# Kernel tuning notes

Hardware: AMD Instinct MI355X
Metric: run time of the kernel (lower is better)

The kernel has to match this reference:

```python
import jax, jax.numpy as jnp
import numpy as np

B, C, N = 8, 512, 2048
C2 = C // 2
BN_EPS = 1e-5


def setup_inputs() -> dict:
    key = jax.random.key(0)
    ks = jax.random.split(key, 8)
    s = lambda fan_in: 1.0 / np.sqrt(fan_in)
    return {
        "q": jax.random.normal(ks[0], (B, C, N), jnp.float32),
        "x": jax.random.normal(ks[1], (B, C2, N), jnp.float32),
        "Wq": jax.random.normal(ks[2], (C2, C), jnp.float32) * s(C),
        "Wk": jax.random.normal(ks[3], (C2, C2), jnp.float32) * s(C2),
        "Wv": jax.random.normal(ks[4], (C2, C), jnp.float32) * s(C),
        "bv": jax.random.normal(ks[5], (C2,), jnp.float32) * 0.01,
        "Wt": jax.random.normal(ks[6], (C2, C2), jnp.float32) * s(C2),
        "bt": jax.random.normal(ks[7], (C2,), jnp.float32) * 0.01,
        "gamma": jnp.ones((C2,), jnp.float32),
        "beta": jnp.zeros((C2,), jnp.float32),
        "running_mean": jnp.zeros((C2,), jnp.float32),
        "running_var": jnp.ones((C2,), jnp.float32),
    }


def reference(q, x, Wq, Wk, Wv, bv, Wt, bt, gamma, beta, running_mean, running_var):
    # 1x1 convs are pointwise GEMMs over the channel dim
    x_q = jnp.einsum("oc,bcn->bno", Wq, q)                    # [B, N, C2]
    x_k = jnp.einsum("oc,bcn->bon", Wk, x)                    # [B, C2, N]
    x_v = jnp.einsum("oc,bcn->bon", Wv, q) + bv[None, :, None]  # [B, C2, N]
    energy = jnp.einsum("bnc,bcm->bnm", x_q, x_k)             # [B, N, N]
    attn = jax.nn.softmax(energy, axis=-1)
    # offset-attention L1 renormalization over the query axis (dim=1)
    attn = attn / (1e-9 + attn.sum(axis=1, keepdims=True))
    x_r = jnp.einsum("bcn,bnm->bcm", x_v, attn)               # [B, C2, N]
    h = jnp.einsum("oc,bcn->bon", Wt, x - x_r) + bt[None, :, None]
    # BatchNorm1d in eval mode with running statistics
    inv = gamma / jnp.sqrt(running_var + BN_EPS)
    h = h * inv[None, :, None] + (beta - running_mean * inv)[None, :, None]
    return jax.nn.relu(h) + x
```

## Files before the change

kernel.cpp:

```cpp
#include <hip/hip_runtime.h>
#include <cstdint>
#include <cstddef>

#define KB_  8
#define KC_  512
#define KC2_ 256
#define KN_  2048

typedef __attribute__((ext_vector_type(8))) __bf16 bf16x8;
typedef __attribute__((ext_vector_type(8))) unsigned short u16x8;
typedef __attribute__((ext_vector_type(4))) float f32x4;

__device__ __forceinline__ unsigned short f2bf(float f) {
  union { float f; unsigned u; } x; x.f = f;
  unsigned r = x.u + 0x7fffu + ((x.u >> 16) & 1u);
  return (unsigned short)(r >> 16);
}
__device__ __forceinline__ float bf2f(unsigned short h) {
  union { unsigned u; float f; } x; x.u = ((unsigned)h) << 16;
  return x.f;
}

#define GLD16(g, l) __builtin_amdgcn_global_load_lds( \
    (__attribute__((address_space(1))) void*)(g),     \
    (__attribute__((address_space(3))) void*)(l), 16, 0, 0)

#define WAIT_VM8()  asm volatile("s_waitcnt vmcnt(8)" ::: "memory")
#define WAIT_VM0()  asm volatile("s_waitcnt vmcnt(0)" ::: "memory")
#define BARRIER()   __builtin_amdgcn_s_barrier()

__device__ __forceinline__ void xcd_swizzle(int& bx, int& by, int& bz) {
  const int gx = gridDim.x, gy = gridDim.y;
  const int nb = gx * gy * (int)gridDim.z;
  int f = ((int)blockIdx.z * gy + (int)blockIdx.y) * gx + (int)blockIdx.x;
  if ((nb & 7) == 0) f = (f & 7) * (nb >> 3) + (f >> 3);
  const int gxy = gx * gy;
  bz = f / gxy; int rem = f - bz * gxy;
  by = rem / gx; bx = rem - by * gx;
}

__global__ __launch_bounds__(256) void cvt_all_kernel(
    const float* __restrict__ Wq, const float* __restrict__ Wk,
    const float* __restrict__ Wv, const float* __restrict__ Wt,
    unsigned short* __restrict__ Wqhi, unsigned short* __restrict__ Wqlo,
    unsigned short* __restrict__ Wkhi, unsigned short* __restrict__ Wklo,
    unsigned short* __restrict__ Wvb, unsigned short* __restrict__ Wtb) {
  int blk = blockIdx.x, t = threadIdx.x;
  if (blk < 128) {
    int i = (blk * 256 + t) * 4;
    float4 f = *(const float4*)(Wq + i);
    ushort4 h = { f2bf(f.x), f2bf(f.y), f2bf(f.z), f2bf(f.w) };
    ushort4 l = { f2bf(f.x - bf2f(h.x)), f2bf(f.y - bf2f(h.y)),
                  f2bf(f.z - bf2f(h.z)), f2bf(f.w - bf2f(h.w)) };
    *(ushort4*)(Wqhi + i) = h; *(ushort4*)(Wqlo + i) = l;
  } else if (blk < 192) {
    int i = ((blk - 128) * 256 + t) * 4;
    float4 f = *(const float4*)(Wk + i);
    ushort4 h = { f2bf(f.x), f2bf(f.y), f2bf(f.z), f2bf(f.w) };
    ushort4 l = { f2bf(f.x - bf2f(h.x)), f2bf(f.y - bf2f(h.y)),
                  f2bf(f.z - bf2f(h.z)), f2bf(f.w - bf2f(h.w)) };
    *(ushort4*)(Wkhi + i) = h; *(ushort4*)(Wklo + i) = l;
  } else if (blk < 320) {
    int i = ((blk - 192) * 256 + t) * 4;
    float4 f = *(const float4*)(Wv + i);
    ushort4 u = { f2bf(f.x), f2bf(f.y), f2bf(f.z), f2bf(f.w) };
    *(ushort4*)(Wvb + i) = u;
  } else {
    int i = ((blk - 320) * 256 + t) * 4;
    float4 f = *(const float4*)(Wt + i);
    ushort4 u = { f2bf(f.x), f2bf(f.y), f2bf(f.z), f2bf(f.w) };
    *(ushort4*)(Wtb + i) = u;
  }
}

__global__ __launch_bounds__(256) void transpose2_kernel(
    const float* __restrict__ q, const float* __restrict__ x,
    unsigned short* __restrict__ qThi, unsigned short* __restrict__ qTlo,
    unsigned short* __restrict__ xThi, unsigned short* __restrict__ xTlo) {
  int b = blockIdx.z;
  const float* in; unsigned short *hi, *lo; int R, r0;
  if (blockIdx.y < 8) {
    in = q + (size_t)b * KC_ * KN_;  hi = qThi; lo = qTlo;
    R = KC_;  r0 = blockIdx.y * 64;
    hi += (size_t)b * KN_ * KC_;  lo += (size_t)b * KN_ * KC_;
  } else {
    in = x + (size_t)b * KC2_ * KN_; hi = xThi; lo = xTlo;
    R = KC2_; r0 = (blockIdx.y - 8) * 64;
    hi += (size_t)b * KN_ * KC2_; lo += (size_t)b * KN_ * KC2_;
  }
  __shared__ float tile[64][65];
  int t = threadIdx.x;
  int c0 = blockIdx.x * 64;
#pragma unroll
  for (int k = 0; k < 4; k++) {
    int vi = k * 256 + t, rr = vi >> 4, cv = vi & 15;
    float4 f = *(const float4*)&in[(size_t)(r0 + rr) * KN_ + c0 + cv * 4];
    tile[rr][cv * 4 + 0] = f.x; tile[rr][cv * 4 + 1] = f.y;
    tile[rr][cv * 4 + 2] = f.z; tile[rr][cv * 4 + 3] = f.w;
  }
  __syncthreads();
#pragma unroll
  for (int k = 0; k < 4; k++) {
    int vi = k * 256 + t, cc = vi >> 4, rv = vi & 15;
    float f0 = tile[rv * 4 + 0][cc], f1 = tile[rv * 4 + 1][cc];
    float f2 = tile[rv * 4 + 2][cc], f3 = tile[rv * 4 + 3][cc];
    ushort4 h = { f2bf(f0), f2bf(f1), f2bf(f2), f2bf(f3) };
    ushort4 l = { f2bf(f0 - bf2f(h.x)), f2bf(f1 - bf2f(h.y)),
                  f2bf(f2 - bf2f(h.z)), f2bf(f3 - bf2f(h.w)) };
    size_t o = (size_t)(c0 + cc) * R + r0 + rv * 4;
    *(ushort4*)&hi[o] = h;
    *(ushort4*)&lo[o] = l;
  }
}

__global__ __launch_bounds__(256) void rowreduce_kernel(const float* __restrict__ rowpart,
                                                        float* __restrict__ rsv) {
  int idx = blockIdx.x * 256 + threadIdx.x;
  const float* p = rowpart + (size_t)idx * 32;
  float s = 0.f;
#pragma unroll
  for (int k = 0; k < 32; k++) s += p[k];
  rsv[idx] = 1.0f / s;
}

__global__ __launch_bounds__(256) void denom_kernel(const unsigned short* __restrict__ uT,
                                                    const float* __restrict__ rsv,
                                                    float* __restrict__ denom) {
  int b = blockIdx.y;
  int m = blockIdx.x * 4 + (threadIdx.x >> 6);
  int lane = threadIdx.x & 63;
  const unsigned short* U = uT + ((size_t)b * KN_ + m) * KN_;
  const float* R = rsv + (size_t)b * KN_;
  float s = 0.f;
#pragma unroll
  for (int c = 0; c < 4; c++) {
    int n = c * 512 + lane * 8;
    u16x8 u = *(const u16x8*)&U[n];
    float4 r0 = *(const float4*)&R[n];
    float4 r1 = *(const float4*)&R[n + 4];
    s += bf2f(u[0]) * r0.x + bf2f(u[1]) * r0.y + bf2f(u[2]) * r0.z + bf2f(u[3]) * r0.w;
    s += bf2f(u[4]) * r1.x + bf2f(u[5]) * r1.y + bf2f(u[6]) * r1.z + bf2f(u[7]) * r1.w;
  }
#pragma unroll
  for (int o = 32; o > 0; o >>= 1) s += __shfl_xor(s, o, 64);
  if (lane == 0) denom[(size_t)b * KN_ + m] = s;
}

__global__ __launch_bounds__(256) void energy_kernel(
    const unsigned short* __restrict__ Ahi, const unsigned short* __restrict__ Alo,
    const unsigned short* __restrict__ Bhi, const unsigned short* __restrict__ Blo,
    unsigned short* __restrict__ uT, float* __restrict__ rowpart) {
  int bx, by, b;
  xcd_swizzle(bx, by, b);
  Ahi += (size_t)b * KN_ * KC2_; Alo += (size_t)b * KN_ * KC2_;
  Bhi += (size_t)b * KN_ * KC2_; Blo += (size_t)b * KN_ * KC2_;
  const int m0 = by * 128;
  const int n0 = bx * 128;
  __shared__ __align__(16) char smem[65536];
  const int t = threadIdx.x, lane = t & 63, w = t >> 6;
  const int wr = w >> 1, wc = w & 1;
  const int srow = t >> 2;
  const int scol = (((t & 3) ^ ((srow >> 1) & 3)) * 8);
  const int lr = lane & 15, lk = (lane >> 4) * 8;
  const int rsw = ((lr >> 1) & 3) << 4;

  auto STAGE = [&](char* dst, int kt) {
    const size_t ga = (size_t)(m0 + srow) * KC2_ + kt + scol;
    const size_t gb = (size_t)(n0 + srow) * KC2_ + kt + scol;
    GLD16(Ahi + ga, dst + 0 + w * 1024);
    GLD16(Ahi + ga + (size_t)64 * KC2_, dst + 4096 + w * 1024);
    GLD16(Alo + ga, dst + 8192 + w * 1024);
    GLD16(Alo + ga + (size_t)64 * KC2_, dst + 12288 + w * 1024);
    GLD16(Bhi + gb, dst + 16384 + w * 1024);
    GLD16(Bhi + gb + (size_t)64 * KC2_, dst + 20480 + w * 1024);
    GLD16(Blo + gb, dst + 24576 + w * 1024);
    GLD16(Blo + gb + (size_t)64 * KC2_, dst + 28672 + w * 1024);
  };

  f32x4 acc[4][4];
  const f32x4 z = {0.f, 0.f, 0.f, 0.f};
#pragma unroll
  for (int i = 0; i < 4; i++)
#pragma unroll
    for (int j = 0; j < 4; j++) acc[i][j] = z;

  STAGE(smem, 0);
  for (int kt8 = 0; kt8 < 8; kt8++) {
    char* cur = smem + (kt8 & 1) * 32768;
    char* nxt = smem + ((kt8 & 1) ^ 1) * 32768;
    if (kt8 < 7) {
      STAGE(nxt, (kt8 + 1) * 32);
      WAIT_VM8();
    } else {
      WAIT_VM0();
    }
    BARRIER();
    bf16x8 ah[4], al[4], bh[4], bl[4];
#pragma unroll
    for (int i = 0; i < 4; i++) {
      int ro = (wr * 64 + i * 16 + lr) * 64 + ((lk * 2) ^ rsw);
      ah[i] = *(const bf16x8*)(cur + 0 + ro);
      al[i] = *(const bf16x8*)(cur + 8192 + ro);
    }
#pragma unroll
    for (int j = 0; j < 4; j++) {
      int ro = (wc * 64 + j * 16 + lr) * 64 + ((lk * 2) ^ rsw);
      bh[j] = *(const bf16x8*)(cur + 16384 + ro);
      bl[j] = *(const bf16x8*)(cur + 24576 + ro);
    }
    __builtin_amdgcn_s_setprio(1);
#pragma unroll
    for (int i = 0; i < 4; i++)
#pragma unroll
      for (int j = 0; j < 4; j++) {
        acc[i][j] = __builtin_amdgcn_mfma_f32_16x16x32_bf16(al[i], bh[j], acc[i][j], 0, 0, 0);
        acc[i][j] = __builtin_amdgcn_mfma_f32_16x16x32_bf16(ah[i], bl[j], acc[i][j], 0, 0, 0);
        acc[i][j] = __builtin_amdgcn_mfma_f32_16x16x32_bf16(ah[i], bh[j], acc[i][j], 0, 0, 0);
      }
    __builtin_amdgcn_s_setprio(0);
    BARRIER();
  }

#pragma unroll
  for (int i = 0; i < 4; i++)
#pragma unroll
    for (int j = 0; j < 4; j++)
#pragma unroll
      for (int r = 0; r < 4; r++) acc[i][j][r] = __expf(acc[i][j][r] - 40.f);

#pragma unroll
  for (int i = 0; i < 4; i++) {
#pragma unroll
    for (int r = 0; r < 4; r++) {
      float s = acc[i][0][r] + acc[i][1][r] + acc[i][2][r] + acc[i][3][r];
      s += __shfl_xor(s, 1, 64); s += __shfl_xor(s, 2, 64);
      s += __shfl_xor(s, 4, 64); s += __shfl_xor(s, 8, 64);
      if ((lane & 15) == 0) {
        int row = m0 + wr * 64 + i * 16 + ((lane >> 4) << 2) + r;
        rowpart[((size_t)b * KN_ + row) * 32 + bx * 2 + wc] = s;
      }
    }
  }

#pragma unroll
  for (int i = 0; i < 4; i++) {
#pragma unroll
    for (int j = 0; j < 4; j++) {
#pragma unroll
      for (int r2 = 0; r2 < 4; r2 += 2) {
        int qn = wr * 64 + i * 16 + ((lane >> 4) << 2) + r2;
        int km = wc * 64 + j * 16 + lr;
        unsigned pk = (unsigned)f2bf(acc[i][j][r2]) |
                      ((unsigned)f2bf(acc[i][j][r2 + 1]) << 16);
        int a = ((km << 8) + (qn << 1)) ^ ((km & 15) << 4);
        *(unsigned*)(smem + a) = pk;
      }
    }
  }
  __syncthreads();
#pragma unroll
  for (int it = 0; it < 8; it++) {
    int km = (t >> 4) + it * 16, chunk = t & 15;
    int a = ((km << 8) + (chunk << 4)) ^ ((km & 15) << 4);
    size_t g = ((size_t)b * KN_ + (n0 + km)) * KN_ + m0 + chunk * 8;
    *(bf16x8*)&uT[g] = *(const bf16x8*)(smem + a);
  }
}

enum { EPI_PAIR = 0, EPI_VSCALE = 2, EPI_XRT = 3, EPI_FINAL = 4 };

struct EpiParams {
  const float* bias;
  const float* xf;  long xf_stride;
  const float* scale; long scale_stride;
  const float* gamma; const float* beta; const float* mean; const float* var;
};

template<int EPI>
__device__ __forceinline__ void gemm_core(
    char* __restrict__ smem, int bx, int by, int b,
    const unsigned short* __restrict__ A0, const unsigned short* __restrict__ A1,
    long sA, int lda, int seg,
    const unsigned short* __restrict__ B0, const unsigned short* __restrict__ B1,
    long sB, int ldb,
    void* __restrict__ Cv, void* __restrict__ Cv2, long sC, int ldc, int K,
    const EpiParams& ep) {
  A0 += (size_t)b * sA; A1 += (size_t)b * sA;
  B0 += (size_t)b * sB; B1 += (size_t)b * sB;
  const int m0 = by * 128, n0 = bx * 128;
  const int t = threadIdx.x, lane = t & 63, w = t >> 6;
  const int wr = w >> 1, wc = w & 1;
  const int srow = t >> 2;
  const int scol = (((t & 3) ^ ((srow >> 1) & 3)) * 8);
  const int lr = lane & 15, lk = (lane >> 4) * 8;
  const int rsw = ((lr >> 1) & 3) << 4;

  auto STAGE = [&](char* dst, int kt) {
    int s = seg ? ((kt >= seg) + (kt >= 2 * seg)) : 0;
    int kl = kt - s * seg;
    const unsigned short* Ab = (s == 1) ? A1 : A0;
    const unsigned short* Bb = (s == 2) ? B1 : B0;
    const unsigned short* gA = Ab + (size_t)(m0 + srow) * lda + kl + scol;
    const unsigned short* gB = Bb + (size_t)(n0 + srow) * ldb + kl + scol;
    GLD16(gA, dst + w * 1024);
    GLD16(gA + (size_t)64 * lda, dst + 4096 + w * 1024);
    GLD16(gA + 32, dst + 8192 + w * 1024);
    GLD16(gA + (size_t)64 * lda + 32, dst + 12288 + w * 1024);
    GLD16(gB, dst + 16384 + w * 1024);
    GLD16(gB + (size_t)64 * ldb, dst + 20480 + w * 1024);
    GLD16(gB + 32, dst + 24576 + w * 1024);
    GLD16(gB + (size_t)64 * ldb + 32, dst + 28672 + w * 1024);
  };

  f32x4 acc[4][4];
  const f32x4 z = {0.f, 0.f, 0.f, 0.f};
#pragma unroll
  for (int i = 0; i < 4; i++)
#pragma unroll
    for (int j = 0; j < 4; j++) acc[i][j] = z;

  const int nt = K >> 6;
  STAGE(smem, 0);
  for (int t8 = 0; t8 < nt; t8++) {
    char* cur = smem + (t8 & 1) * 32768;
    char* nxt = smem + ((t8 & 1) ^ 1) * 32768;
    if (t8 < nt - 1) {
      STAGE(nxt, (t8 + 1) * 64);
      WAIT_VM8();
    } else {
      WAIT_VM0();
    }
    BARRIER();
#pragma unroll
    for (int kk = 0; kk < 2; kk++) {
      bf16x8 af[4], bfv[4];
#pragma unroll
      for (int i = 0; i < 4; i++)
        af[i] = *(const bf16x8*)(cur + kk * 8192 +
                                 (wr * 64 + i * 16 + lr) * 64 + ((lk * 2) ^ rsw));
#pragma unroll
      for (int j = 0; j < 4; j++)
        bfv[j] = *(const bf16x8*)(cur + 16384 + kk * 8192 +
                                  (wc * 64 + j * 16 + lr) * 64 + ((lk * 2) ^ rsw));
#pragma unroll
      for (int i = 0; i < 4; i++)
#pragma unroll
        for (int j = 0; j < 4; j++)
          acc[i][j] = __builtin_amdgcn_mfma_f32_16x16x32_bf16(af[i], bfv[j], acc[i][j], 0, 0, 0);
    }
    BARRIER();
  }

  if constexpr (EPI == EPI_XRT) {
    float dinv[4];
#pragma unroll
    for (int j = 0; j < 4; j++)
      dinv[j] = 1.0f / (1e-9f + ep.scale[(size_t)b * ep.scale_stride +
                                         n0 + wc * 64 + j * 16 + lr]);
    const float* X = ep.xf + (size_t)b * ep.xf_stride;
#pragma unroll
    for (int i = 0; i < 4; i++) {
#pragma unroll
      for (int j = 0; j < 4; j++) {
#pragma unroll
        for (int r2 = 0; r2 < 4; r2 += 2) {
          int cl = wr * 64 + i * 16 + ((lane >> 4) << 2) + r2;
          int ml = wc * 64 + j * 16 + lr;
          float x0 = X[(size_t)(m0 + cl) * KN_ + n0 + ml];
          float x1 = X[(size_t)(m0 + cl + 1) * KN_ + n0 + ml];
          float t0 = x0 - acc[i][j][r2] * dinv[j];
          float t1 = x1 - acc[i][j][r2 + 1] * dinv[j];
          unsigned pk = (unsigned)f2bf(t0) | ((unsigned)f2bf(t1) << 16);
          int a = ((ml << 8) + (cl << 1)) ^ ((ml & 15) << 4);
          *(unsigned*)(smem + a) = pk;
        }
      }
    }
    __syncthreads();
    unsigned short* tT = (unsigned short*)Cv;
#pragma unroll
    for (int it = 0; it < 8; it++) {
      int ml = (t >> 4) + it * 16, chunk = t & 15;
      int a = ((ml << 8) + (chunk << 4)) ^ ((ml & 15) << 4);
      size_t g = ((size_t)b * KN_ + (n0 + ml)) * KC2_ + m0 + chunk * 8;
      *(bf16x8*)&tT[g] = *(const bf16x8*)(smem + a);
    }
    return;
  }

#pragma unroll
  for (int i = 0; i < 4; i++) {
#pragma unroll
    for (int r = 0; r < 4; r++) {
      const int row = m0 + wr * 64 + i * 16 + ((lane >> 4) << 2) + r;
      float pbias = 0.f, pinv = 1.f, padd = 0.f;
      if constexpr (EPI == EPI_VSCALE) pbias = ep.bias[row];
      if constexpr (EPI == EPI_FINAL) {
        pbias = ep.bias[row];
        float iv = ep.gamma[row] * rsqrtf(ep.var[row] + 1e-5f);
        pinv = iv;
        padd = ep.beta[row] - ep.mean[row] * iv;
      }
#pragma unroll
      for (int j = 0; j < 4; j++) {
        const int col = n0 + wc * 64 + j * 16 + lr;
        float v = acc[i][j][r];
        size_t o = (size_t)b * sC + (size_t)row * ldc + col;
        if constexpr (EPI == EPI_PAIR) {
          unsigned short h = f2bf(v);
          ((unsigned short*)Cv)[o] = h;
          ((unsigned short*)Cv2)[o] = f2bf(v - bf2f(h));
        } else if constexpr (EPI == EPI_VSCALE) {
          float sc = ep.scale[(size_t)b * ep.scale_stride + col];
          ((unsigned short*)Cv)[o] = f2bf((v + pbias) * sc);
        } else {
          float h = (v + pbias) * pinv + padd;
          h = fmaxf(h, 0.f);
          float xval = ep.xf[(size_t)b * ep.xf_stride + o - (size_t)b * sC];
          ((float*)Cv)[o] = h + xval;
        }
      }
    }
  }
}

template<int EPI>
__global__ __launch_bounds__(256) void gemm_one(
    const unsigned short* __restrict__ A0, const unsigned short* __restrict__ A1,
    long sA, int lda, int seg,
    const unsigned short* __restrict__ B0, const unsigned short* __restrict__ B1,
    long sB, int ldb,
    void* __restrict__ Cv, void* __restrict__ Cv2, long sC, int ldc, int K,
    EpiParams ep) {
  __shared__ __align__(16) char smem[65536];
  int bx, by, b;
  xcd_swizzle(bx, by, b);
  gemm_core<EPI>(smem, bx, by, b, A0, A1, sA, lda, seg, B0, B1, sB, ldb,
                 Cv, Cv2, sC, ldc, K, ep);
}

__global__ __launch_bounds__(256) void proj2_kernel(
    const unsigned short* __restrict__ qThi, const unsigned short* __restrict__ qTlo,
    const unsigned short* __restrict__ Wqhi, const unsigned short* __restrict__ Wqlo,
    unsigned short* __restrict__ xqhi, unsigned short* __restrict__ xqlo,
    const unsigned short* __restrict__ xThi, const unsigned short* __restrict__ xTlo,
    const unsigned short* __restrict__ Wkhi, const unsigned short* __restrict__ Wklo,
    unsigned short* __restrict__ xkhi, unsigned short* __restrict__ xklo) {
  __shared__ __align__(16) char smem[65536];
  int f = (int)blockIdx.x;
  f = (f & 7) * 64 + (f >> 3);
  EpiParams ep{};
  if (f < 256) {
    int bx = f & 1, by = (f >> 1) & 15, b = f >> 5;
    gemm_core<EPI_PAIR>(smem, bx, by, b, qThi, qTlo, (long)KN_ * KC_, KC_, KC_,
                        Wqhi, Wqlo, 0, KC_, xqhi, xqlo, (long)KN_ * KC2_, KC2_,
                        3 * KC_, ep);
  } else {
    int g = f - 256;
    int bx = g & 1, by = (g >> 1) & 15, b = g >> 5;
    gemm_core<EPI_PAIR>(smem, bx, by, b, xThi, xTlo, (long)KN_ * KC2_, KC2_, KC2_,
                        Wkhi, Wklo, 0, KC2_, xkhi, xklo, (long)KN_ * KC2_, KC2_,
                        3 * KC2_, ep);
  }
}

extern "C" void kernel_launch(void* const* d_in, const int* in_sizes, int n_in,
                              void* d_out, int out_size, void* d_ws, size_t ws_size,
                              hipStream_t stream) {
  (void)in_sizes; (void)n_in; (void)out_size; (void)ws_size;
  const float* q     = (const float*)d_in[0];
  const float* x     = (const float*)d_in[1];
  const float* Wq    = (const float*)d_in[2];
  const float* Wk    = (const float*)d_in[3];
  const float* Wv    = (const float*)d_in[4];
  const float* bv    = (const float*)d_in[5];
  const float* Wt    = (const float*)d_in[6];
  const float* bt    = (const float*)d_in[7];
  const float* gamma = (const float*)d_in[8];
  const float* beta  = (const float*)d_in[9];
  const float* rmean = (const float*)d_in[10];
  const float* rvar  = (const float*)d_in[11];
  float* out = (float*)d_out;

  const size_t SZ_qT = (size_t)KB_ * KN_ * KC_ * 2;
  const size_t SZ_xT = (size_t)KB_ * KN_ * KC2_ * 2;
  char* ws = (char*)d_ws;
  size_t off = 0;
  auto alloc = [&](size_t bytes) {
    char* p = ws + off;
    off += (bytes + 255) & ~(size_t)255;
    return p;
  };
  unsigned short* qThi = (unsigned short*)alloc(SZ_qT);
  unsigned short* qTlo = (unsigned short*)alloc(SZ_qT);
  unsigned short* xThi = (unsigned short*)alloc(SZ_xT);
  unsigned short* xTlo = (unsigned short*)alloc(SZ_xT);
  unsigned short* xqhi = (unsigned short*)alloc(SZ_xT);
  unsigned short* xqlo = (unsigned short*)alloc(SZ_xT);
  unsigned short* xkhi = (unsigned short*)alloc(SZ_xT);
  unsigned short* xklo = (unsigned short*)alloc(SZ_xT);
  unsigned short* x_v  = (unsigned short*)alloc((size_t)KB_ * KC2_ * KN_ * 2);
  unsigned short* tT   = (unsigned short*)alloc(SZ_xT);
  unsigned short* Wqhi = (unsigned short*)alloc((size_t)KC2_ * KC_ * 2);
  unsigned short* Wqlo = (unsigned short*)alloc((size_t)KC2_ * KC_ * 2);
  unsigned short* Wkhi = (unsigned short*)alloc((size_t)KC2_ * KC2_ * 2);
  unsigned short* Wklo = (unsigned short*)alloc((size_t)KC2_ * KC2_ * 2);
  unsigned short* Wvb  = (unsigned short*)alloc((size_t)KC2_ * KC_ * 2);
  unsigned short* Wtb  = (unsigned short*)alloc((size_t)KC2_ * KC2_ * 2);
  float* rsv     = (float*)alloc((size_t)KB_ * KN_ * 4);
  float* denom   = (float*)alloc((size_t)KB_ * KN_ * 4);
  float* rowpart = (float*)alloc((size_t)KB_ * KN_ * 32 * 4);
  unsigned short* uT = (unsigned short*)alloc((size_t)KB_ * KN_ * KN_ * 2);

  dim3 blk(256);

  cvt_all_kernel<<<dim3(384), blk, 0, stream>>>(Wq, Wk, Wv, Wt,
                                                Wqhi, Wqlo, Wkhi, Wklo, Wvb, Wtb);

  transpose2_kernel<<<dim3(KN_ / 64, 12, KB_), blk, 0, stream>>>(
      q, x, qThi, qTlo, xThi, xTlo);

  proj2_kernel<<<dim3(512), blk, 0, stream>>>(qThi, qTlo, Wqhi, Wqlo, xqhi, xqlo,
                                              xThi, xTlo, Wkhi, Wklo, xkhi, xklo);

  energy_kernel<<<dim3(KN_ / 128, KN_ / 128, KB_), blk, 0, stream>>>(
      xqhi, xqlo, xkhi, xklo, uT, rowpart);
  rowreduce_kernel<<<dim3(KB_ * KN_ / 256), blk, 0, stream>>>(rowpart, rsv);

  EpiParams e3{}; e3.bias = bv; e3.scale = rsv; e3.scale_stride = KN_;
  gemm_one<EPI_VSCALE><<<dim3(KN_ / 128, KC2_ / 128, KB_), blk, 0, stream>>>(
      Wvb, nullptr, 0, KC_, 0, qThi, nullptr, (long)KN_ * KC_, KC_,
      x_v, nullptr, (long)KC2_ * KN_, KN_, KC_, e3);

  denom_kernel<<<dim3(KN_ / 4, KB_), blk, 0, stream>>>(uT, rsv, denom);

  EpiParams e5{}; e5.xf = x; e5.xf_stride = (long)KC2_ * KN_;
  e5.scale = denom; e5.scale_stride = KN_;
  gemm_one<EPI_XRT><<<dim3(KN_ / 128, KC2_ / 128, KB_), blk, 0, stream>>>(
      x_v, nullptr, (long)KC2_ * KN_, KN_, 0, uT, nullptr, (long)KN_ * KN_, KN_,
      tT, nullptr, 0, 0, KN_, e5);

  EpiParams e6{}; e6.bias = bt; e6.xf = x; e6.xf_stride = (long)KC2_ * KN_;
  e6.gamma = gamma; e6.beta = beta; e6.mean = rmean; e6.var = rvar;
  gemm_one<EPI_FINAL><<<dim3(KN_ / 128, KC2_ / 128, KB_), blk, 0, stream>>>(
      Wtb, nullptr, 0, KC2_, 0, tT, nullptr, (long)KN_ * KC2_, KC2_,
      out, nullptr, (long)KC2_ * KN_, KN_, KC2_, e6);
}
```

Baseline: 191.3 us.

## Fuse attention column-denominator into XRT GEMM mainloop and drop denom kernel

Removes the standalone denom kernel, which re-read the full bf16 attention matrix, and instead accumulates the dot product of each B-tile column with the reciprocal row sums inside the XRT GEMM main loop, reducing across lanes in the epilogue. This saves a full pass over the large uT buffer and one launch, at the cost of extra VALU work per K-step and redundant computation across channel blocks. Also removes setprio hints around the MFMA block in the energy kernel.

```diff
diff --git a/kernel.cpp b/kernel.cpp
--- a/kernel.cpp
+++ b/kernel.cpp
@@ -123,29 +123,6 @@
   rsv[idx] = 1.0f / s;
 }
 
-__global__ __launch_bounds__(256) void denom_kernel(const unsigned short* __restrict__ uT,
-                                                    const float* __restrict__ rsv,
-                                                    float* __restrict__ denom) {
-  int b = blockIdx.y;
-  int m = blockIdx.x * 4 + (threadIdx.x >> 6);
-  int lane = threadIdx.x & 63;
-  const unsigned short* U = uT + ((size_t)b * KN_ + m) * KN_;
-  const float* R = rsv + (size_t)b * KN_;
-  float s = 0.f;
-#pragma unroll
-  for (int c = 0; c < 4; c++) {
-    int n = c * 512 + lane * 8;
-    u16x8 u = *(const u16x8*)&U[n];
-    float4 r0 = *(const float4*)&R[n];
-    float4 r1 = *(const float4*)&R[n + 4];
-    s += bf2f(u[0]) * r0.x + bf2f(u[1]) * r0.y + bf2f(u[2]) * r0.z + bf2f(u[3]) * r0.w;
-    s += bf2f(u[4]) * r1.x + bf2f(u[5]) * r1.y + bf2f(u[6]) * r1.z + bf2f(u[7]) * r1.w;
-  }
-#pragma unroll
-  for (int o = 32; o > 0; o >>= 1) s += __shfl_xor(s, o, 64);
-  if (lane == 0) denom[(size_t)b * KN_ + m] = s;
-}
-
 __global__ __launch_bounds__(256) void energy_kernel(
     const unsigned short* __restrict__ Ahi, const unsigned short* __restrict__ Alo,
     const unsigned short* __restrict__ Bhi, const unsigned short* __restrict__ Blo,
@@ -208,7 +185,6 @@
       bh[j] = *(const bf16x8*)(cur + 16384 + ro);
       bl[j] = *(const bf16x8*)(cur + 24576 + ro);
     }
-    __builtin_amdgcn_s_setprio(1);
 #pragma unroll
     for (int i = 0; i < 4; i++)
 #pragma unroll
@@ -217,7 +193,6 @@
         acc[i][j] = __builtin_amdgcn_mfma_f32_16x16x32_bf16(ah[i], bl[j], acc[i][j], 0, 0, 0);
         acc[i][j] = __builtin_amdgcn_mfma_f32_16x16x32_bf16(ah[i], bh[j], acc[i][j], 0, 0, 0);
       }
-    __builtin_amdgcn_s_setprio(0);
     BARRIER();
   }
 
@@ -273,6 +248,7 @@
   const float* bias;
   const float* xf;  long xf_stride;
   const float* scale; long scale_stride;
+  const float* rsvp;
   const float* gamma; const float* beta; const float* mean; const float* var;
 };
 
@@ -318,6 +294,7 @@
   for (int i = 0; i < 4; i++)
 #pragma unroll
     for (int j = 0; j < 4; j++) acc[i][j] = z;
+  float ddot[4] = {0.f, 0.f, 0.f, 0.f};
 
   const int nt = K >> 6;
   STAGE(smem, 0);
@@ -342,6 +319,18 @@
       for (int j = 0; j < 4; j++)
         bfv[j] = *(const bf16x8*)(cur + 16384 + kk * 8192 +
                                   (wc * 64 + j * 16 + lr) * 64 + ((lk * 2) ^ rsw));
+      if constexpr (EPI == EPI_XRT) {
+        const float* Rv = ep.rsvp + (size_t)b * KN_ + t8 * 64 + kk * 32 + lk;
+        float4 r0 = *(const float4*)Rv;
+        float4 r1 = *(const float4*)(Rv + 4);
+#pragma unroll
+        for (int j = 0; j < 4; j++) {
+          ddot[j] += (float)bfv[j][0] * r0.x + (float)bfv[j][1] * r0.y +
+                     (float)bfv[j][2] * r0.z + (float)bfv[j][3] * r0.w +
+                     (float)bfv[j][4] * r1.x + (float)bfv[j][5] * r1.y +
+                     (float)bfv[j][6] * r1.z + (float)bfv[j][7] * r1.w;
+        }
+      }
 #pragma unroll
       for (int i = 0; i < 4; i++)
 #pragma unroll
@@ -354,9 +343,12 @@
   if constexpr (EPI == EPI_XRT) {
     float dinv[4];
 #pragma unroll
-    for (int j = 0; j < 4; j++)
-      dinv[j] = 1.0f / (1e-9f + ep.scale[(size_t)b * ep.scale_stride +
-                                         n0 + wc * 64 + j * 16 + lr]);
+    for (int j = 0; j < 4; j++) {
+      float d = ddot[j];
+      d += __shfl_xor(d, 16, 64);
+      d += __shfl_xor(d, 32, 64);
+      dinv[j] = 1.0f / (1e-9f + d);
+    }
     const float* X = ep.xf + (size_t)b * ep.xf_stride;
 #pragma unroll
     for (int i = 0; i < 4; i++) {
@@ -508,7 +500,6 @@
   unsigned short* Wvb  = (unsigned short*)alloc((size_t)KC2_ * KC_ * 2);
   unsigned short* Wtb  = (unsigned short*)alloc((size_t)KC2_ * KC2_ * 2);
   float* rsv     = (float*)alloc((size_t)KB_ * KN_ * 4);
-  float* denom   = (float*)alloc((size_t)KB_ * KN_ * 4);
   float* rowpart = (float*)alloc((size_t)KB_ * KN_ * 32 * 4);
   unsigned short* uT = (unsigned short*)alloc((size_t)KB_ * KN_ * KN_ * 2);
 
@@ -532,10 +523,8 @@
       Wvb, nullptr, 0, KC_, 0, qThi, nullptr, (long)KN_ * KC_, KC_,
       x_v, nullptr, (long)KC2_ * KN_, KN_, KC_, e3);
 
-  denom_kernel<<<dim3(KN_ / 4, KB_), blk, 0, stream>>>(uT, rsv, denom);
-
   EpiParams e5{}; e5.xf = x; e5.xf_stride = (long)KC2_ * KN_;
-  e5.scale = denom; e5.scale_stride = KN_;
+  e5.rsvp = rsv;
   gemm_one<EPI_XRT><<<dim3(KN_ / 128, KC2_ / 128, KB_), blk, 0, stream>>>(
       x_v, nullptr, (long)KC2_ * KN_, KN_, 0, uT, nullptr, (long)KN_ * KN_, KN_,
       tT, nullptr, 0, 0, KN_, e5);
```

Measured after the change: 189.0 us, median of 2. Within noise of the previous version (-1.2%).
